# Optimization experiments

Measured on AMD Instinct MI355X. Metric: run time of the kernel, lower is better.

Reference implementation:

```python
import jax, jax.numpy as jnp
import numpy as np

GROUP_SIZE = 128  # QuantizationConfig default


def setup_inputs() -> dict:
    key = jax.random.key(0)
    k0, k1, k2, k3 = jax.random.split(key, 4)
    B, IN, OUT = 32, 4096, 16384
    NG = IN // GROUP_SIZE  # 32 groups
    x = jax.random.normal(k0, (B, IN), dtype=jnp.float16)
    # int8 symmetric-quantized weights in [-127, 127]
    qweight = jax.random.randint(k1, (OUT, IN), -127, 128, dtype=jnp.int8)
    # per-(out_channel, group) fp16 scales; small positive values as produced by absmax/127
    scales = (jax.random.uniform(k2, (OUT, NG), dtype=jnp.float16) * jnp.float16(0.01)
              + jnp.float16(1e-3))
    bias = jax.random.normal(k3, (OUT,), dtype=jnp.float16) * jnp.float16(0.01)
    return {"x": x, "qweight": qweight, "scales": scales, "bias": bias}


def reference(x, qweight, scales, bias):
    # QuantizedLinear._forward_grouped, sym=True, in_features % group_size == 0 path.
    OUT, IN = qweight.shape
    NG = IN // GROUP_SIZE
    # dequantize: [OUT, NG, G] * [OUT, NG, 1] -> [OUT, IN], all in fp16
    w_deq = (qweight.astype(jnp.float16).reshape(OUT, NG, GROUP_SIZE)
             * scales[:, :, None]).reshape(OUT, IN)
    # F.linear(x, w_deq) = x @ w_deq.T, then + bias
    out = jnp.dot(x, w_deq.T) + bias
    return out
```

## Files before the change

kernel.cpp:

```cpp
#include <hip/hip_runtime.h>

typedef __attribute__((ext_vector_type(8))) short short8;
typedef __attribute__((ext_vector_type(4))) float f32x4;
typedef __attribute__((ext_vector_type(4))) int   i32x4;

#define IN_F   4096
#define OUT_F  16384
#define NG     32
#define BK     64
#define NCH    32

static __device__ __forceinline__ short f2bf(float f) {
    union { float f; unsigned u; } c; c.f = f;
    unsigned u = c.u;
    u += 0x7FFF + ((u >> 16) & 1);
    return (short)(u >> 16);
}

static __device__ __forceinline__ short i2bf(int v) {
    union { float f; unsigned u; } c; c.f = (float)v;
    return (short)(c.u >> 16);
}

__global__ __launch_bounds__(256)
void xconv_kernel(const float* __restrict__ x, unsigned short* __restrict__ xT) {
    const int g   = blockIdx.x * 256 + threadIdx.x;
    const int t   = g >> 7;
    const int rem = g & 127;
    const int h   = rem >> 6;
    const int ln  = rem & 63;
    const int l15 = ln >> 2;
    const int l4  = ln & 3;
    const float* src = x + (size_t)(16 * h + l15) * IN_F + t * 32 + l4 * 8;
    f32x4 a = *(const f32x4*)src;
    f32x4 b = *(const f32x4*)(src + 4);
    short8 o;
#pragma unroll
    for (int j = 0; j < 4; ++j) { o[j] = f2bf(a[j]); o[j + 4] = f2bf(b[j]); }
    *(short8*)(xT + (size_t)g * 8) = o;
}

__global__ __launch_bounds__(512, 4)
void qlin_kernel(const unsigned short* __restrict__ xT,
                 const int*   __restrict__ qw,
                 const float* __restrict__ scales,
                 const float* __restrict__ bias,
                 float*       __restrict__ out)
{
    __shared__ int lqw[2][4][32][BK];

    const int tid  = threadIdx.x;
    const int wv   = tid >> 6;
    const int lane = tid & 63;
    const int l15  = lane & 15;
    const int l4   = lane >> 4;
    const int wk   = wv >> 2;
    const int wm   = (wv >> 1) & 1;
    const int wn   = wv & 1;
    const int widx = wv & 3;
    const int col0 = blockIdx.x * 32;

    const int rowB = 16 * wn + l15;
    const int swzB = (rowB & 7) << 4;

    auto STAGE = [&](int c, int sl) {
        const size_t kbase = (size_t)wk * 2048 + (size_t)c * BK;
#pragma unroll
        for (int i = 0; i < 2; ++i) {
            const int p   = widx * 2 + i;
            const int row = 4 * p + (lane >> 4);
            const int byt = ((lane & 15) * 16) ^ ((row & 7) << 4);
            const char* src = (const char*)(qw + (size_t)(col0 + row) * IN_F + kbase) + byt;
            __builtin_amdgcn_global_load_lds(
                (const __attribute__((address_space(1))) unsigned int*)src,
                (__attribute__((address_space(3))) unsigned int*)&lqw[wk][sl][4 * p][0],
                16, 0, 0);
        }
    };

    const unsigned short* xgrp = xT + (size_t)(l15 * 4 + l4) * 8 + (size_t)wm * 512;
    short8 xa[2][2];
    auto XLOAD = [&](int c, int par) {
        const int t = wk * 64 + c * 2;
        xa[par][0] = *(const short8*)(xgrp + (size_t)t * 1024);
        xa[par][1] = *(const short8*)(xgrp + (size_t)(t + 1) * 1024);
    };

    const float* scr = scales + (size_t)(col0 + rowB) * NG + wk * 16;
    f32x4 sc4[4];
#pragma unroll
    for (int j = 0; j < 4; ++j) sc4[j] = *(const f32x4*)(scr + 4 * j);

    f32x4 acc = {0.f, 0.f, 0.f, 0.f};

    auto COMPUTE = [&](int c, int sl, int par, float sc) {
        const char* lrow = (const char*)&lqw[wk][sl][rowB][0];
        f32x4 ag = {0.f, 0.f, 0.f, 0.f};
#pragma unroll
        for (int s = 0; s < 2; ++s) {
            const int byte0 = (s * 128 + l4 * 32) ^ swzB;
            i32x4 q0 = *(const i32x4*)(lrow + byte0);
            i32x4 q1 = *(const i32x4*)(lrow + (byte0 ^ 16));
            short8 bfr;
#pragma unroll
            for (int j = 0; j < 4; ++j) { bfr[j] = i2bf(q0[j]); bfr[j + 4] = i2bf(q1[j]); }
            ag = __builtin_amdgcn_mfma_f32_16x16x32_bf16(xa[par][s], bfr, ag, 0, 0, 0);
        }
#pragma unroll
        for (int r = 0; r < 4; ++r) acc[r] += sc * ag[r];
    };

    STAGE(0, 0);
    asm volatile("" ::: "memory");
    XLOAD(0, 0);
    XLOAD(1, 1);
    asm volatile("" ::: "memory");
    STAGE(1, 1);
    STAGE(2, 2);
    asm volatile("s_waitcnt vmcnt(6)" ::: "memory");
    __builtin_amdgcn_s_barrier();
    __builtin_amdgcn_sched_barrier(0);

#pragma unroll
    for (int i = 0; i <= 28; ++i) {
        COMPUTE(i, i & 3, i & 1, sc4[i >> 3][(i >> 1) & 3]);
        XLOAD(i + 2, i & 1);
        asm volatile("" ::: "memory");
        STAGE(i + 3, (i + 3) & 3);
        asm volatile("s_waitcnt vmcnt(6)" ::: "memory");
        __builtin_amdgcn_s_barrier();
        __builtin_amdgcn_sched_barrier(0);
    }
    COMPUTE(29, 1, 1, sc4[3][2]);
    XLOAD(31, 1);
    asm volatile("s_waitcnt vmcnt(4)" ::: "memory");
    __builtin_amdgcn_s_barrier();
    __builtin_amdgcn_sched_barrier(0);
    COMPUTE(30, 2, 0, sc4[3][3]);
    asm volatile("s_waitcnt vmcnt(0)" ::: "memory");
    __builtin_amdgcn_s_barrier();
    __builtin_amdgcn_sched_barrier(0);
    COMPUTE(31, 3, 1, sc4[3][3]);

    __syncthreads();
    float* red = (float*)&lqw[0][0][0][0];
    *(f32x4*)&red[(size_t)(wv * 64 + lane) * 4] = acc;
    __syncthreads();
    if (wv < 4) {
        const int col = col0 + rowB;
        const float bv = bias[col];
        f32x4 lo = *(const f32x4*)&red[(size_t)(wv * 64 + lane) * 4];
        f32x4 hi = *(const f32x4*)&red[(size_t)((wv + 4) * 64 + lane) * 4];
#pragma unroll
        for (int r = 0; r < 4; ++r)
            out[(size_t)(16 * wm + l4 * 4 + r) * OUT_F + col] = lo[r] + hi[r] + bv;
    }
}

extern "C" void kernel_launch(void* const* d_in, const int* in_sizes, int n_in,
                              void* d_out, int out_size, void* d_ws, size_t ws_size,
                              hipStream_t stream) {
    const float* x      = (const float*)d_in[0];
    const int*   qw     = (const int*)d_in[1];
    const float* scales = (const float*)d_in[2];
    const float* bias   = (const float*)d_in[3];
    float*       out    = (float*)d_out;
    unsigned short* xT  = (unsigned short*)d_ws;

    hipLaunchKernelGGL(xconv_kernel, dim3(64), dim3(256), 0, stream, x, xT);
    hipLaunchKernelGGL(qlin_kernel, dim3(OUT_F / 32), dim3(512), 0, stream,
                       xT, qw, scales, bias, out);
}
```

Before: 53.05 us.

## Give each wave private weight tiles covering both M halves, drop block barriers

Each block now covers 64 output columns, and each wave stages its own 16-row weight slice into a private LDS region. Each wave runs two MFMAs against both 16-row halves of x, so a dequantized weight fragment is converted once and reused for all 32 batch rows instead of being duplicated across waves. Because staging is wave-private, the per-chunk s_barrier is removed and only vmcnt waits remain. The cost is twice the LDS per block, more x registers per wave, half the grid size and a lower occupancy bound.

```diff
diff --git a/kernel.cpp b/kernel.cpp
--- a/kernel.cpp
+++ b/kernel.cpp
@@ -7,7 +7,6 @@
 #define IN_F   4096
 #define OUT_F  16384
 #define NG     32
-#define BK     64
 #define NCH    32
 
 static __device__ __forceinline__ short f2bf(float f) {
@@ -40,85 +39,89 @@
     *(short8*)(xT + (size_t)g * 8) = o;
 }
 
-__global__ __launch_bounds__(512, 4)
+__global__ __launch_bounds__(512, 2)
 void qlin_kernel(const unsigned short* __restrict__ xT,
                  const int*   __restrict__ qw,
                  const float* __restrict__ scales,
                  const float* __restrict__ bias,
                  float*       __restrict__ out)
 {
-    __shared__ int lqw[2][4][32][BK];
+    __shared__ int lqw[8][4][16][64];
 
     const int tid  = threadIdx.x;
     const int wv   = tid >> 6;
     const int lane = tid & 63;
     const int l15  = lane & 15;
     const int l4   = lane >> 4;
-    const int wk   = wv >> 2;
-    const int wm   = (wv >> 1) & 1;
-    const int wn   = wv & 1;
-    const int widx = wv & 3;
-    const int col0 = blockIdx.x * 32;
+    const int grp  = wv >> 1;
+    const int wk   = wv & 1;
+    const int col0 = blockIdx.x * 64 + grp * 16;
+    const int swz  = (l15 & 7) << 4;
 
-    const int rowB = 16 * wn + l15;
-    const int swzB = (rowB & 7) << 4;
+    const float* scr = scales + (size_t)(col0 + l15) * NG + wk * 16;
+    f32x4 sc4[4];
+#pragma unroll
+    for (int j = 0; j < 4; ++j) sc4[j] = *(const f32x4*)(scr + 4 * j);
+    const float bv = bias[col0 + l15];
+    asm volatile("" ::: "memory");
 
     auto STAGE = [&](int c, int sl) {
-        const size_t kbase = (size_t)wk * 2048 + (size_t)c * BK;
 #pragma unroll
-        for (int i = 0; i < 2; ++i) {
-            const int p   = widx * 2 + i;
-            const int row = 4 * p + (lane >> 4);
+        for (int i = 0; i < 4; ++i) {
+            const int row = 4 * i + (lane >> 4);
             const int byt = ((lane & 15) * 16) ^ ((row & 7) << 4);
-            const char* src = (const char*)(qw + (size_t)(col0 + row) * IN_F + kbase) + byt;
+            const char* src = (const char*)(qw + (size_t)(col0 + row) * IN_F
+                                            + wk * 2048 + c * 64) + byt;
             __builtin_amdgcn_global_load_lds(
                 (const __attribute__((address_space(1))) unsigned int*)src,
-                (__attribute__((address_space(3))) unsigned int*)&lqw[wk][sl][4 * p][0],
+                (__attribute__((address_space(3))) unsigned int*)&lqw[wv][sl][4 * i][0],
                 16, 0, 0);
         }
     };
 
-    const unsigned short* xgrp = xT + (size_t)(l15 * 4 + l4) * 8 + (size_t)wm * 512;
-    short8 xa[2][2];
+    const unsigned short* xg = xT + (size_t)(l15 * 4 + l4) * 8;
+    short8 xa[2][2][2];
     auto XLOAD = [&](int c, int par) {
-        const int t = wk * 64 + c * 2;
-        xa[par][0] = *(const short8*)(xgrp + (size_t)t * 1024);
-        xa[par][1] = *(const short8*)(xgrp + (size_t)(t + 1) * 1024);
+        const int t0 = wk * 64 + c * 2;
+#pragma unroll
+        for (int s = 0; s < 2; ++s)
+#pragma unroll
+            for (int h = 0; h < 2; ++h)
+                xa[par][s][h] = *(const short8*)(xg + (size_t)((t0 + s) * 2 + h) * 512);
     };
 
-    const float* scr = scales + (size_t)(col0 + rowB) * NG + wk * 16;
-    f32x4 sc4[4];
-#pragma unroll
-    for (int j = 0; j < 4; ++j) sc4[j] = *(const f32x4*)(scr + 4 * j);
-
-    f32x4 acc = {0.f, 0.f, 0.f, 0.f};
+    f32x4 acc[2] = {{0.f, 0.f, 0.f, 0.f}, {0.f, 0.f, 0.f, 0.f}};
 
     auto COMPUTE = [&](int c, int sl, int par, float sc) {
-        const char* lrow = (const char*)&lqw[wk][sl][rowB][0];
-        f32x4 ag = {0.f, 0.f, 0.f, 0.f};
+        const char* lrow = (const char*)&lqw[wv][sl][l15][0];
+        f32x4 ag[2] = {{0.f, 0.f, 0.f, 0.f}, {0.f, 0.f, 0.f, 0.f}};
 #pragma unroll
         for (int s = 0; s < 2; ++s) {
-            const int byte0 = (s * 128 + l4 * 32) ^ swzB;
-            i32x4 q0 = *(const i32x4*)(lrow + byte0);
-            i32x4 q1 = *(const i32x4*)(lrow + (byte0 ^ 16));
+            const int off = (s * 128 + l4 * 32) ^ swz;
+            i32x4 q0 = *(const i32x4*)(lrow + off);
+            i32x4 q1 = *(const i32x4*)(lrow + (off ^ 16));
             short8 bfr;
 #pragma unroll
             for (int j = 0; j < 4; ++j) { bfr[j] = i2bf(q0[j]); bfr[j + 4] = i2bf(q1[j]); }
-            ag = __builtin_amdgcn_mfma_f32_16x16x32_bf16(xa[par][s], bfr, ag, 0, 0, 0);
+            ag[0] = __builtin_amdgcn_mfma_f32_16x16x32_bf16(xa[par][s][0], bfr, ag[0], 0, 0, 0);
+            ag[1] = __builtin_amdgcn_mfma_f32_16x16x32_bf16(xa[par][s][1], bfr, ag[1], 0, 0, 0);
         }
 #pragma unroll
-        for (int r = 0; r < 4; ++r) acc[r] += sc * ag[r];
+        for (int h = 0; h < 2; ++h)
+#pragma unroll
+            for (int r = 0; r < 4; ++r) acc[h][r] += sc * ag[h][r];
     };
 
     STAGE(0, 0);
     asm volatile("" ::: "memory");
     XLOAD(0, 0);
+    asm volatile("" ::: "memory");
+    STAGE(1, 1);
+    asm volatile("" ::: "memory");
     XLOAD(1, 1);
     asm volatile("" ::: "memory");
-    STAGE(1, 1);
     STAGE(2, 2);
-    asm volatile("s_waitcnt vmcnt(6)" ::: "memory");
-    __builtin_amdgcn_s_barrier();
+    asm volatile("s_waitcnt vmcnt(12)" ::: "memory");
     __builtin_amdgcn_sched_barrier(0);
 
 #pragma unroll
@@ -127,33 +130,33 @@
         XLOAD(i + 2, i & 1);
         asm volatile("" ::: "memory");
         STAGE(i + 3, (i + 3) & 3);
-        asm volatile("s_waitcnt vmcnt(6)" ::: "memory");
-        __builtin_amdgcn_s_barrier();
+        asm volatile("s_waitcnt vmcnt(12)" ::: "memory");
         __builtin_amdgcn_sched_barrier(0);
     }
     COMPUTE(29, 1, 1, sc4[3][2]);
     XLOAD(31, 1);
-    asm volatile("s_waitcnt vmcnt(4)" ::: "memory");
-    __builtin_amdgcn_s_barrier();
+    asm volatile("s_waitcnt vmcnt(8)" ::: "memory");
     __builtin_amdgcn_sched_barrier(0);
     COMPUTE(30, 2, 0, sc4[3][3]);
     asm volatile("s_waitcnt vmcnt(0)" ::: "memory");
-    __builtin_amdgcn_s_barrier();
     __builtin_amdgcn_sched_barrier(0);
     COMPUTE(31, 3, 1, sc4[3][3]);
 
     __syncthreads();
     float* red = (float*)&lqw[0][0][0][0];
-    *(f32x4*)&red[(size_t)(wv * 64 + lane) * 4] = acc;
+#pragma unroll
+    for (int h = 0; h < 2; ++h)
+        *(f32x4*)&red[(size_t)(((wv * 64 + lane) * 2) + h) * 4] = acc[h];
     __syncthreads();
-    if (wv < 4) {
-        const int col = col0 + rowB;
-        const float bv = bias[col];
-        f32x4 lo = *(const f32x4*)&red[(size_t)(wv * 64 + lane) * 4];
-        f32x4 hi = *(const f32x4*)&red[(size_t)((wv + 4) * 64 + lane) * 4];
+    if (wk == 0) {
 #pragma unroll
-        for (int r = 0; r < 4; ++r)
-            out[(size_t)(16 * wm + l4 * 4 + r) * OUT_F + col] = lo[r] + hi[r] + bv;
+        for (int h = 0; h < 2; ++h) {
+            f32x4 hi = *(const f32x4*)&red[(size_t)((((wv + 1) * 64 + lane) * 2) + h) * 4];
+#pragma unroll
+            for (int r = 0; r < 4; ++r)
+                out[(size_t)(h * 16 + l4 * 4 + r) * OUT_F + col0 + l15] =
+                    acc[h][r] + hi[r] + bv;
+        }
     }
 }
 
@@ -168,6 +171,6 @@
     unsigned short* xT  = (unsigned short*)d_ws;
 
     hipLaunchKernelGGL(xconv_kernel, dim3(64), dim3(256), 0, stream, x, xT);
-    hipLaunchKernelGGL(qlin_kernel, dim3(OUT_F / 32), dim3(512), 0, stream,
+    hipLaunchKernelGGL(qlin_kernel, dim3(OUT_F / 64), dim3(512), 0, stream,
                        xT, qw, scales, bias, out);
 }
```

Result: faster. 51.90 us (median of 2 runs) (-2.2%).
